# Kernel tuning notes

Hardware: AMD Instinct MI355X
Metric: run time of the kernel (lower is better)

The kernel has to match this reference:

```python
import jax, jax.numpy as jnp
import numpy as np

CUTOFF = 1.0  # nm
KE = 138.96   # Coulomb constant conversion factor used by the module


def physnet_attenuation(r, cutoff=CUTOFF):
    # PhysNet smooth switching function: 1 - 6u^5 + 15u^4 - 10u^3 for u<1, else 0
    u = r / cutoff
    phi = 1.0 - 6.0 * u**5 + 15.0 * u**4 - 10.0 * u**3
    return jnp.where(u < 1.0, phi, 0.0)


def setup_inputs() -> dict:
    key = jax.random.key(0)
    k1, k2, k3, k4 = jax.random.split(key, 4)
    N = 262144          # total atoms
    P = 16777216        # total pairs (~64 neighbors/atom)
    S = 1024            # number of systems
    pair_idx = jax.random.randint(k1, (2, P), 0, N, dtype=jnp.int32)
    # distances in (0.05, 1.25) nm; 2*d straddles the cutoff so both branches of chi_r are exercised
    d_ij = (jax.random.uniform(k2, (P, 1), dtype=jnp.float32) * 1.2 + 0.05)
    charge = jax.random.normal(k3, (N, 1), dtype=jnp.float32) * 0.3
    sys_idx = jnp.sort(jax.random.randint(k4, (N,), 0, S, dtype=jnp.int32))
    return {
        "electrostatic_pair_indices": pair_idx,
        "electrostatic_d_ij": d_ij,
        "per_atom_charge": charge,
        "atomic_subsystem_indices": sys_idx,
        "num_systems": S,
    }


def reference(electrostatic_pair_indices, electrostatic_d_ij, per_atom_charge,
              atomic_subsystem_indices, num_systems):
    idx_i = electrostatic_pair_indices[0]
    idx_j = electrostatic_pair_indices[1]
    # unique-pair mask (static shapes: zero out instead of filtering)
    mask = idx_i < idx_j
    d = electrostatic_d_ij[:, 0]                       # [P]
    q = per_atom_charge[:, 0]                          # [N]
    phi_2r = physnet_attenuation(2.0 * d)
    chi_r = phi_2r / jnp.sqrt(d * d + 1.0) + (1.0 - phi_2r) / d
    e_pair = q[idx_i] * q[idx_j] * chi_r               # [P]
    e_pair = jnp.where(mask, e_pair, 0.0)
    seg = atomic_subsystem_indices[idx_i]              # system of each pair
    per_system = jax.ops.segment_sum(e_pair, seg, num_segments=num_systems)
    return (per_system * KE)[:, None]                  # [S, 1]
```

## Files before the change

### kernel.cpp

```cpp
#include <hip/hip_runtime.h>

typedef int   v4i __attribute__((ext_vector_type(4)));
typedef float v4f __attribute__((ext_vector_type(4)));

#define S_SYS   1024
#define KE_CONST 138.96f
#define BLOCKS  1024
#define THREADS 256

__global__ __launch_bounds__(256) void pack_kernel(const float* __restrict__ q,
                                                   const int* __restrict__ sys,
                                                   float2* __restrict__ packed, int N) {
    int i = blockIdx.x * blockDim.x + threadIdx.x;
    if (i < N) {
        float2 v;
        v.x = q[i];
        v.y = __int_as_float(sys[i]);
        packed[i] = v;
    }
}

__global__ __launch_bounds__(256) void pair_kernel(const v4i* __restrict__ idx_i4,
                                                   const v4i* __restrict__ idx_j4,
                                                   const v4f* __restrict__ d4,
                                                   const float2* __restrict__ packed,
                                                   float* __restrict__ partial,
                                                   int P4) {
    __shared__ float acc[4][S_SYS];
    const int tid = threadIdx.x;
    const int wave = tid >> 6;
    for (int t = tid; t < 4 * S_SYS; t += THREADS) ((float*)acc)[t] = 0.0f;
    __syncthreads();

    const int stride = gridDim.x * blockDim.x;
    for (int p = blockIdx.x * blockDim.x + tid; p < P4; p += stride) {
        v4i vi = __builtin_nontemporal_load(&idx_i4[p]);
        v4i vj = __builtin_nontemporal_load(&idx_j4[p]);
        v4f vd = __builtin_nontemporal_load(&d4[p]);
#pragma unroll
        for (int k = 0; k < 4; ++k) {
            int i = vi[k], j = vj[k];
            if (i < j) {
                float d  = vd[k];
                float2 pi = packed[i];
                float qj  = packed[j].x;
                float u = 2.0f * d;
                float phi = 0.0f;
                if (u < 1.0f) {
                    float u3 = u * u * u;
                    phi = 1.0f - u3 * (10.0f + u * (6.0f * u - 15.0f));
                }
                float chi = phi * __builtin_amdgcn_rsqf(d * d + 1.0f)
                          + (1.0f - phi) * __builtin_amdgcn_rcpf(d);
                float e = pi.x * qj * chi;
                atomicAdd(&acc[wave][__float_as_int(pi.y)], e);
            }
        }
    }
    __syncthreads();
    for (int s = tid; s < S_SYS; s += THREADS) {
        float v = acc[0][s] + acc[1][s] + acc[2][s] + acc[3][s];
        partial[(size_t)blockIdx.x * S_SYS + s] = v;
    }
}

__global__ __launch_bounds__(256) void reduce_kernel(const float* __restrict__ partial,
                                                     float* __restrict__ out, int B) {
    int s = blockIdx.x;
    float sum = 0.0f;
    for (int b = threadIdx.x; b < B; b += blockDim.x)
        sum += partial[(size_t)b * S_SYS + s];
#pragma unroll
    for (int off = 32; off > 0; off >>= 1) sum += __shfl_down(sum, off, 64);
    __shared__ float wsum[4];
    if ((threadIdx.x & 63) == 0) wsum[threadIdx.x >> 6] = sum;
    __syncthreads();
    if (threadIdx.x == 0) out[s] = KE_CONST * (wsum[0] + wsum[1] + wsum[2] + wsum[3]);
}

extern "C" void kernel_launch(void* const* d_in, const int* in_sizes, int n_in,
                              void* d_out, int out_size, void* d_ws, size_t ws_size,
                              hipStream_t stream) {
    const int*   pair = (const int*)d_in[0];
    const float* d_ij = (const float*)d_in[1];
    const float* q    = (const float*)d_in[2];
    const int*   sys  = (const int*)d_in[3];
    const int P = in_sizes[1];
    const int N = in_sizes[2];
    float* out = (float*)d_out;

    float2* packed  = (float2*)d_ws;
    float*  partial = (float*)((char*)d_ws + (size_t)N * sizeof(float2));

    pack_kernel<<<(N + 255) / 256, 256, 0, stream>>>(q, sys, packed, N);

    pair_kernel<<<BLOCKS, THREADS, 0, stream>>>(
        (const v4i*)pair, (const v4i*)(pair + P), (const v4f*)d_ij,
        packed, partial, P / 4);

    reduce_kernel<<<S_SYS, 256, 0, stream>>>(partial, out, BLOCKS);
}
```

Baseline: 302.8 us.

## Software-pipeline pair loads, batch gathers, double grid, coalesce reduction with atomics

The pair kernel now prefetches the next iteration's index and distance vectors while processing the current one, and issues all four charge gathers before doing the math. The grid is doubled to 2048 blocks with an occupancy hint of 8 blocks per CU. The reduction is restructured so each thread sums a contiguous chunk of per-block partials for one system, reading coalesced across threads, and atomically adds into an output that is zeroed beforehand. This trades more partial rows and register pressure for better latency hiding, plus an extra memset and global atomics.

Result: no change. 304.8 us (+0.7%).

```diff
diff --git a/kernel.cpp b/kernel.cpp
--- a/kernel.cpp
+++ b/kernel.cpp
@@ -3,10 +3,11 @@
 typedef int   v4i __attribute__((ext_vector_type(4)));
 typedef float v4f __attribute__((ext_vector_type(4)));
 
-#define S_SYS   1024
+#define S_SYS    1024
 #define KE_CONST 138.96f
-#define BLOCKS  1024
-#define THREADS 256
+#define BLOCKS   2048
+#define THREADS  256
+#define RBLOCKS  256
 
 __global__ __launch_bounds__(256) void pack_kernel(const float* __restrict__ q,
                                                    const int* __restrict__ sys,
@@ -20,12 +21,12 @@
     }
 }
 
-__global__ __launch_bounds__(256) void pair_kernel(const v4i* __restrict__ idx_i4,
-                                                   const v4i* __restrict__ idx_j4,
-                                                   const v4f* __restrict__ d4,
-                                                   const float2* __restrict__ packed,
-                                                   float* __restrict__ partial,
-                                                   int P4) {
+__global__ __launch_bounds__(256, 8) void pair_kernel(const v4i* __restrict__ idx_i4,
+                                                      const v4i* __restrict__ idx_j4,
+                                                      const v4f* __restrict__ d4,
+                                                      const float2* __restrict__ packed,
+                                                      float* __restrict__ partial,
+                                                      int P4) {
     __shared__ float acc[4][S_SYS];
     const int tid = threadIdx.x;
     const int wave = tid >> 6;
@@ -33,28 +34,50 @@
     __syncthreads();
 
     const int stride = gridDim.x * blockDim.x;
-    for (int p = blockIdx.x * blockDim.x + tid; p < P4; p += stride) {
+    int p = blockIdx.x * blockDim.x + tid;
+
+    if (p < P4) {
         v4i vi = __builtin_nontemporal_load(&idx_i4[p]);
         v4i vj = __builtin_nontemporal_load(&idx_j4[p]);
         v4f vd = __builtin_nontemporal_load(&d4[p]);
+        for (;;) {
+            const int pn = p + stride;
+            const bool more = pn < P4;
+            v4i nvi, nvj; v4f nvd;
+            if (more) {
+                nvi = __builtin_nontemporal_load(&idx_i4[pn]);
+                nvj = __builtin_nontemporal_load(&idx_j4[pn]);
+                nvd = __builtin_nontemporal_load(&d4[pn]);
+            }
+            bool  m[4];
+            float2 pi[4];
+            float  qj[4];
 #pragma unroll
-        for (int k = 0; k < 4; ++k) {
-            int i = vi[k], j = vj[k];
-            if (i < j) {
-                float d  = vd[k];
-                float2 pi = packed[i];
-                float qj  = packed[j].x;
-                float u = 2.0f * d;
-                float phi = 0.0f;
-                if (u < 1.0f) {
-                    float u3 = u * u * u;
-                    phi = 1.0f - u3 * (10.0f + u * (6.0f * u - 15.0f));
+            for (int k = 0; k < 4; ++k) {
+                m[k] = vi[k] < vj[k];
+                if (m[k]) {
+                    pi[k] = packed[vi[k]];
+                    qj[k] = packed[vj[k]].x;
                 }
-                float chi = phi * __builtin_amdgcn_rsqf(d * d + 1.0f)
-                          + (1.0f - phi) * __builtin_amdgcn_rcpf(d);
-                float e = pi.x * qj * chi;
-                atomicAdd(&acc[wave][__float_as_int(pi.y)], e);
             }
+#pragma unroll
+            for (int k = 0; k < 4; ++k) {
+                if (m[k]) {
+                    float d = vd[k];
+                    float u = 2.0f * d;
+                    float phi = 0.0f;
+                    if (u < 1.0f) {
+                        float u3 = u * u * u;
+                        phi = 1.0f - u3 * (10.0f + u * (6.0f * u - 15.0f));
+                    }
+                    float chi = phi * __builtin_amdgcn_rsqf(d * d + 1.0f)
+                              + (1.0f - phi) * __builtin_amdgcn_rcpf(d);
+                    float e = pi[k].x * qj[k] * chi;
+                    atomicAdd(&acc[wave][__float_as_int(pi[k].y)], e);
+                }
+            }
+            if (!more) break;
+            vi = nvi; vj = nvj; vd = nvd; p = pn;
         }
     }
     __syncthreads();
@@ -66,16 +89,16 @@
 
 __global__ __launch_bounds__(256) void reduce_kernel(const float* __restrict__ partial,
                                                      float* __restrict__ out, int B) {
-    int s = blockIdx.x;
+    const int sgroup = blockIdx.x & 3;
+    const int chunk  = blockIdx.x >> 2;
+    const int nchunk = gridDim.x >> 2;
+    const int s = sgroup * 256 + threadIdx.x;
+    const int bpc = B / nchunk;
+    const int b0 = chunk * bpc;
     float sum = 0.0f;
-    for (int b = threadIdx.x; b < B; b += blockDim.x)
+    for (int b = b0; b < b0 + bpc; ++b)
         sum += partial[(size_t)b * S_SYS + s];
-#pragma unroll
-    for (int off = 32; off > 0; off >>= 1) sum += __shfl_down(sum, off, 64);
-    __shared__ float wsum[4];
-    if ((threadIdx.x & 63) == 0) wsum[threadIdx.x >> 6] = sum;
-    __syncthreads();
-    if (threadIdx.x == 0) out[s] = KE_CONST * (wsum[0] + wsum[1] + wsum[2] + wsum[3]);
+    atomicAdd(&out[s], KE_CONST * sum);
 }
 
 extern "C" void kernel_launch(void* const* d_in, const int* in_sizes, int n_in,
@@ -92,11 +115,13 @@
     float2* packed  = (float2*)d_ws;
     float*  partial = (float*)((char*)d_ws + (size_t)N * sizeof(float2));
 
+    hipMemsetAsync(out, 0, (size_t)out_size * sizeof(float), stream);
+
     pack_kernel<<<(N + 255) / 256, 256, 0, stream>>>(q, sys, packed, N);
 
     pair_kernel<<<BLOCKS, THREADS, 0, stream>>>(
         (const v4i*)pair, (const v4i*)(pair + P), (const v4f*)d_ij,
         packed, partial, P / 4);
 
-    reduce_kernel<<<S_SYS, 256, 0, stream>>>(partial, out, BLOCKS);
+    reduce_kernel<<<RBLOCKS, 256, 0, stream>>>(partial, out, BLOCKS);
 }
```
